# Optimization experiments

Hardware: AMD Instinct MI355X
Metric: run time of the kernel (lower is better)

## Reference

```python
import jax, jax.numpy as jnp
import numpy as np

D_MODEL = 192
DEPTH = 16
D_INNER = 384   # expand=2
D_STATE = 16
D_CONV = 4
DT_RANK = 12    # ceil(192/16)
J = 42
T = 8
NUM_CLASSES = 1000
B = 64
EPS = 1e-5


def setup_inputs() -> dict:
    key = jax.random.key(0)
    ks = jax.random.split(key, 16)

    def n(k, shape, scale=0.02):
        return jax.random.normal(k, shape, jnp.float32) * scale

    dt_bias_init = float(np.log(np.expm1(0.01)))  # softplus^-1(0.01), mamba dt init
    A_init = jnp.log(jnp.tile(jnp.arange(1, D_STATE + 1, dtype=jnp.float32), (DEPTH, D_INNER, 1)))
    return {
        "x": jax.random.normal(ks[0], (B, T, J, 3), jnp.float32),
        "joint_embed_w": n(ks[1], (D_MODEL, 3)),
        "joint_embed_b": jnp.zeros((D_MODEL,), jnp.float32),
        "cls_token": n(ks[2], (1, 1, D_MODEL)),
        "spatial_pos": n(ks[3], (1, J + 1, D_MODEL)),
        "temporal_pos": n(ks[4], (1, T, D_MODEL)),
        "norm_w": jnp.ones((DEPTH, D_MODEL), jnp.float32),
        "in_proj_w": n(ks[5], (DEPTH, 2 * D_INNER, D_MODEL)),
        "conv_w": n(ks[6], (DEPTH, D_INNER, D_CONV), 0.1),
        "conv_b": jnp.zeros((DEPTH, D_INNER), jnp.float32),
        "x_proj_w": n(ks[7], (DEPTH, DT_RANK + 2 * D_STATE, D_INNER)),
        "dt_proj_w": n(ks[8], (DEPTH, D_INNER, DT_RANK), DT_RANK ** -0.5),
        "dt_proj_b": jnp.full((DEPTH, D_INNER), dt_bias_init, jnp.float32),
        "A_log": A_init,
        "Dp": jnp.ones((DEPTH, D_INNER), jnp.float32),
        "out_proj_w": n(ks[9], (DEPTH, D_MODEL, D_INNER)),
        "norm_f_w": jnp.ones((D_MODEL,), jnp.float32),
        "head_w": n(ks[10], (NUM_CLASSES, D_MODEL)),
        "head_b": jnp.zeros((NUM_CLASSES,), jnp.float32),
    }


def rmsnorm(x, w):
    return x * jax.lax.rsqrt(jnp.mean(x * x, axis=-1, keepdims=True) + EPS) * w


def mamba(x, in_w, cw, cb, xp_w, dtw, dtb, A_log, Dp, ow):
    # x: (B, L, d_model)
    Bsz, L, _ = x.shape
    xz = jnp.einsum('bld,ed->ble', x, in_w)          # (B,L,2*di)
    u, z = jnp.split(xz, 2, axis=-1)
    # depthwise causal conv over time
    uc = jnp.transpose(u, (0, 2, 1))                  # (B,di,L)
    uc = jnp.pad(uc, ((0, 0), (0, 0), (D_CONV - 1, 0)))
    uc = jax.lax.conv_general_dilated(
        uc, cw[:, None, :], (1,), 'VALID',
        dimension_numbers=('NCH', 'OIH', 'NCH'),
        feature_group_count=D_INNER) + cb[None, :, None]
    u = jax.nn.silu(jnp.transpose(uc, (0, 2, 1)))     # (B,L,di)
    dbl = jnp.einsum('bld,ed->ble', u, xp_w)          # (B,L,dt_rank+2*ds)
    dt, Bm, Cm = jnp.split(dbl, [DT_RANK, DT_RANK + D_STATE], axis=-1)
    delta = jax.nn.softplus(jnp.einsum('blr,dr->bld', dt, dtw) + dtb)  # (B,L,di)
    A = -jnp.exp(A_log)                               # (di,ds)

    def step(h, xs):
        d_t, B_t, C_t, u_t = xs                       # (B,di),(B,ds),(B,ds),(B,di)
        h = h * jnp.exp(d_t[..., None] * A) + (d_t * u_t)[..., None] * B_t[:, None, :]
        return h, jnp.einsum('bds,bs->bd', h, C_t)

    xs = (jnp.swapaxes(delta, 0, 1), jnp.swapaxes(Bm, 0, 1),
          jnp.swapaxes(Cm, 0, 1), jnp.swapaxes(u, 0, 1))
    h0 = jnp.zeros((Bsz, D_INNER, D_STATE), x.dtype)
    _, ys = jax.lax.scan(step, h0, xs)                # (L,B,di)
    y = jnp.swapaxes(ys, 0, 1) + u * Dp
    y = y * jax.nn.silu(z)
    return jnp.einsum('ble,de->bld', y, ow)


def reference(x, joint_embed_w, joint_embed_b, cls_token, spatial_pos, temporal_pos,
              norm_w, in_proj_w, conv_w, conv_b, x_proj_w, dt_proj_w, dt_proj_b,
              A_log, Dp, out_proj_w, norm_f_w, head_w, head_b):
    Bq, Tq, Jq, _ = x.shape
    xe = jnp.einsum('btjc,dc->btjd', x, joint_embed_w) + joint_embed_b
    xe = xe.reshape(Bq * Tq, Jq, D_MODEL)
    cls = jnp.broadcast_to(cls_token, (Bq * Tq, 1, D_MODEL))
    xcat = jnp.concatenate([cls, xe], axis=1) + spatial_pos   # (B*T, J+1, M)
    cls_tokens = xcat[:Bq, :1, :]
    body = xcat[:, 1:, :].reshape(Bq, Tq, Jq, D_MODEL)
    body = body.transpose(0, 2, 1, 3).reshape(Bq * Jq, Tq, D_MODEL) + temporal_pos
    body = body.reshape(Bq, Jq, Tq, D_MODEL).transpose(0, 2, 1, 3).reshape(Bq, Tq * Jq, D_MODEL)
    h = jnp.concatenate([cls_tokens, body], axis=1)           # (B, 1+T*J, M)

    residual = None
    for i in range(DEPTH):
        residual = h + residual if residual is not None else h
        hn = rmsnorm(residual, norm_w[i])
        h = mamba(hn, in_proj_w[i], conv_w[i], conv_b[i], x_proj_w[i],
                  dt_proj_w[i], dt_proj_b[i], A_log[i], Dp[i], out_proj_w[i])
    residual = h + residual
    feat = rmsnorm(residual, norm_f_w)[:, 0, :]
    return feat @ head_w.T + head_b
```

## Files before the change

kernel.cpp:

```cpp
#include <hip/hip_runtime.h>
#include <hip/hip_bf16.h>
#include <math.h>

#define B_ 64
#define T_ 8
#define J_ 42
#define L_ 337
#define D_ 192
#define E_ 384
#define S_ 16
#define R_ 12
#define DEPTH_ 16
#define NC_ 1000
#define M_ (B_*L_)
#define XZW_ (2*E_)
#define DBLW_ (R_+2*S_)
#define EPS_ 1e-5f
#define CH_ 22
#define NCH_ 16
#define LOG2E_ 1.44269504088896f

typedef float    f32x4  __attribute__((ext_vector_type(4)));
typedef unsigned u32x4  __attribute__((ext_vector_type(4)));
typedef __bf16   bf16x8 __attribute__((ext_vector_type(8)));

__device__ __forceinline__ float sigmoid_(float x){ return 1.f/(1.f+__expf(-x)); }
__device__ __forceinline__ float softplus_(float x){
  return (x > 20.f) ? x : __logf(1.f + __expf(x));
}
__device__ __forceinline__ unsigned short f2bf(float f){
  unsigned u = __float_as_uint(f);
  unsigned r = (u + 0x7fffu + ((u>>16)&1u)) >> 16;
  return (unsigned short)r;
}
__device__ __forceinline__ float bf2f(unsigned short h){
  return __uint_as_float(((unsigned)h)<<16);
}

__global__ void cvt_bf16_kernel(const float* __restrict__ in,
                                unsigned short* __restrict__ out, int n){
  int i = blockIdx.x*blockDim.x + threadIdx.x;
  if (i < n) out[i] = f2bf(in[i]);
}

__global__ void embed_kernel(const float* __restrict__ x,
                             const float* __restrict__ jw,
                             const float* __restrict__ jb,
                             const float* __restrict__ cls,
                             const float* __restrict__ sp,
                             const float* __restrict__ tp,
                             float* __restrict__ h) {
  int idx = blockIdx.x*blockDim.x + threadIdx.x;
  if (idx >= M_*D_) return;
  int d = idx % D_;
  int m = idx / D_;
  int l = m % L_;
  int b = m / L_;
  float v;
  if (l == 0) {
    v = cls[d] + sp[d];
  } else {
    int lm = l-1, t = lm / J_, j = lm % J_;
    const float* xp = x + ((size_t)((b*T_+t)*J_ + j))*3;
    v = jb[d] + sp[(1+j)*D_+d] + tp[t*D_+d]
      + xp[0]*jw[d*3+0] + xp[1]*jw[d*3+1] + xp[2]*jw[d*3+2];
  }
  h[idx] = v;
}

__global__ __launch_bounds__(64) void addnorm_kernel(float* __restrict__ residual,
    const float* __restrict__ h, const float* __restrict__ w,
    unsigned short* __restrict__ hn) {
  int m = blockIdx.x;
  int lane = threadIdx.x;
  size_t base = (size_t)m*D_;
  float r[3];
  float ss = 0.f;
  #pragma unroll
  for (int i=0;i<3;i++){
    int d = lane + i*64;
    r[i] = residual[base+d] + h[base+d];
    residual[base+d] = r[i];
    ss += r[i]*r[i];
  }
  #pragma unroll
  for (int off=32; off>=1; off>>=1) ss += __shfl_xor(ss, off, 64);
  float sc = rsqrtf(ss*(1.f/(float)D_) + EPS_);
  #pragma unroll
  for (int i=0;i<3;i++){
    int d = lane + i*64;
    hn[base+d] = f2bf(r[i]*sc*w[d]);
  }
}

template<int NWAVES>
__global__ __launch_bounds__(64*NWAVES) void gemm_mfma(
    const unsigned short* __restrict__ A,
    const unsigned short* __restrict__ W,
    float* __restrict__ C, int M, int N, int K)
{
  const int wave = threadIdx.x >> 6;
  const int lane = threadIdx.x & 63;
  const int row0 = blockIdx.x * 64;
  const int col0 = (blockIdx.y * NWAVES + wave) * 64;
  const int lr = lane & 15;
  const int lk = (lane >> 4) * 8;
  const bf16x8 bzero = __builtin_bit_cast(bf16x8, (u32x4)(0u));
  f32x4 acc[4][4] = {};
  for (int k0 = 0; k0 < K; k0 += 32) {
    bf16x8 af[4], bfr[4];
    #pragma unroll
    for (int i=0;i<4;i++)
      af[i] = __builtin_bit_cast(bf16x8,
          *(const u32x4*)(A + (size_t)(row0 + i*16 + lr)*K + k0 + lk));
    #pragma unroll
    for (int j=0;j<4;j++) {
      int col = col0 + j*16 + lr;
      bfr[j] = (col < N) ? __builtin_bit_cast(bf16x8,
          *(const u32x4*)(W + (size_t)col*K + k0 + lk)) : bzero;
    }
    #pragma unroll
    for (int i=0;i<4;i++)
      #pragma unroll
      for (int j=0;j<4;j++)
        acc[i][j] = __builtin_amdgcn_mfma_f32_16x16x32_bf16(af[i], bfr[j], acc[i][j], 0, 0, 0);
  }
  const int ro = (lane >> 4) * 4;
  #pragma unroll
  for (int i=0;i<4;i++) {
    #pragma unroll
    for (int j=0;j<4;j++) {
      int col = col0 + j*16 + lr;
      if (col >= N) continue;
      #pragma unroll
      for (int r=0;r<4;r++) {
        int row = row0 + i*16 + ro + r;
        C[(size_t)row*N + col] = acc[i][j][r];
      }
    }
  }
}

__global__ void conv_silu_kernel(const float* __restrict__ xz,
    const float* __restrict__ cw, const float* __restrict__ cb,
    unsigned short* __restrict__ u2) {
  int idx = blockIdx.x*blockDim.x + threadIdx.x;
  if (idx >= M_*E_) return;
  int d = idx % E_;
  int m = idx / E_;
  int l = m % L_;
  float acc = cb[d];
  #pragma unroll
  for (int k=0;k<4;k++){
    int lk = l + k - 3;
    if (lk >= 0) acc += cw[d*4+k] * xz[(size_t)(m + k - 3)*XZW_ + d];
  }
  u2[idx] = f2bf(acc * sigmoid_(acc));
}

__global__ __launch_bounds__(64) void scan_partA(
    const float* __restrict__ dbl,
    const unsigned short* __restrict__ u2,
    const float* __restrict__ dtw,
    const float* __restrict__ dtb,
    const float* __restrict__ A_log,
    float* __restrict__ part_h,
    float* __restrict__ part_sd)
{
  const int b = blockIdx.x;
  const int d = blockIdx.y*64 + threadIdx.x;
  const int c = blockIdx.z;
  const int t0 = c*CH_;
  const int t1 = (t0+CH_ < L_) ? t0+CH_ : L_;
  float dtw_r[R_];
  #pragma unroll
  for (int r=0;r<R_;r++) dtw_r[r] = dtw[d*R_+r];
  const float dtb_r = dtb[d];
  const float a1 = -__expf(A_log[d*S_]) * LOG2E_;
  float h[S_];
  #pragma unroll
  for (int s=0;s<S_;s++) h[s] = 0.f;
  float sum_dl = 0.f;
  const size_t m0 = (size_t)b*L_;

  float4 q[7];
  { const float4* dr = (const float4*)(dbl + (m0+t0)*DBLW_);
    #pragma unroll
    for (int i=0;i<7;i++) q[i] = dr[i]; }
  float u_ = bf2f(u2[(m0+t0)*E_ + d]);

  for (int t=t0; t<t1; ++t) {
    float4 nq[7]; float nu = 0.f;
    if (t+1 < t1) {
      const float4* dr = (const float4*)(dbl + (m0+t+1)*DBLW_);
      #pragma unroll
      for (int i=0;i<7;i++) nq[i] = dr[i];
      nu = bf2f(u2[(m0+t+1)*E_ + d]);
    }
    float qf[28];
    #pragma unroll
    for (int i=0;i<7;i++){
      qf[4*i+0]=q[i].x; qf[4*i+1]=q[i].y; qf[4*i+2]=q[i].z; qf[4*i+3]=q[i].w;
    }
    float dtv = dtb_r;
    #pragma unroll
    for (int r=0;r<R_;r++) dtv = fmaf(qf[r], dtw_r[r], dtv);
    dtv = softplus_(dtv);
    sum_dl += dtv;
    const float du = dtv * u_;
    const float rr = exp2f(dtv * a1);
    float p = rr;
    #pragma unroll
    for (int s=0;s<S_;s++){
      h[s] = fmaf(h[s], p, du*qf[R_+s]);
      p *= rr;
    }
    #pragma unroll
    for (int i=0;i<7;i++) q[i] = nq[i];
    u_ = nu;
  }
  const size_t pb = (size_t)b*NCH_ + c;
  #pragma unroll
  for (int s=0;s<S_;s++) part_h[(pb*S_ + s)*E_ + d] = h[s];
  part_sd[pb*E_ + d] = sum_dl;
}

__global__ __launch_bounds__(64) void scan_partC(
    const float* __restrict__ dbl,
    const unsigned short* __restrict__ u2,
    const float* __restrict__ xz,
    const float* __restrict__ dtw, const float* __restrict__ dtb,
    const float* __restrict__ A_log, const float* __restrict__ Dp,
    const float* __restrict__ part_h, const float* __restrict__ part_sd,
    unsigned short* __restrict__ y)
{
  const int b = blockIdx.x;
  const int d = blockIdx.y*64 + threadIdx.x;
  const int c = blockIdx.z;
  const int t0 = c*CH_;
  const int t1 = (t0+CH_ < L_) ? t0+CH_ : L_;
  float dtw_r[R_];
  #pragma unroll
  for (int r=0;r<R_;r++) dtw_r[r] = dtw[d*R_+r];
  const float dtb_r = dtb[d];
  const float dpv   = Dp[d];
  const float a1 = -__expf(A_log[d*S_]) * LOG2E_;
  float h[S_];
  #pragma unroll
  for (int s=0;s<S_;s++) h[s] = 0.f;
  for (int cc=0; cc<c; ++cc) {
    const size_t pb = (size_t)b*NCH_ + cc;
    const float sd = part_sd[pb*E_ + d];
    const float rr = exp2f(a1*sd);
    float p = rr;
    #pragma unroll
    for (int s=0;s<S_;s++){
      h[s] = fmaf(h[s], p, part_h[(pb*S_ + s)*E_ + d]);
      p *= rr;
    }
  }

  const size_t m0 = (size_t)b*L_;
  float4 q[11];
  { const float4* dr = (const float4*)(dbl + (m0+t0)*DBLW_);
    #pragma unroll
    for (int i=0;i<11;i++) q[i] = dr[i]; }
  float u_ = bf2f(u2[(m0+t0)*E_ + d]);
  float z_ = xz[(m0+t0)*XZW_ + E_ + d];

  for (int t=t0; t<t1; ++t) {
    float4 nq[11]; float nu = 0.f, nz = 0.f;
    if (t+1 < t1) {
      const float4* dr = (const float4*)(dbl + (m0+t+1)*DBLW_);
      #pragma unroll
      for (int i=0;i<11;i++) nq[i] = dr[i];
      nu = bf2f(u2[(m0+t+1)*E_ + d]);
      nz = xz[(m0+t+1)*XZW_ + E_ + d];
    }
    float qf[44];
    #pragma unroll
    for (int i=0;i<11;i++){
      qf[4*i+0]=q[i].x; qf[4*i+1]=q[i].y; qf[4*i+2]=q[i].z; qf[4*i+3]=q[i].w;
    }
    float dtv = dtb_r;
    #pragma unroll
    for (int r=0;r<R_;r++) dtv = fmaf(qf[r], dtw_r[r], dtv);
    dtv = softplus_(dtv);
    const float du = dtv * u_;
    const float rr = exp2f(dtv * a1);
    float p = rr;
    float acc0=0.f, acc1=0.f, acc2=0.f, acc3=0.f;
    #pragma unroll
    for (int s=0;s<S_;s+=4){
      h[s+0] = fmaf(h[s+0], p, du*qf[R_+s+0]); p *= rr;
      h[s+1] = fmaf(h[s+1], p, du*qf[R_+s+1]); p *= rr;
      h[s+2] = fmaf(h[s+2], p, du*qf[R_+s+2]); p *= rr;
      h[s+3] = fmaf(h[s+3], p, du*qf[R_+s+3]); p *= rr;
      acc0 = fmaf(h[s+0], qf[R_+S_+s+0], acc0);
      acc1 = fmaf(h[s+1], qf[R_+S_+s+1], acc1);
      acc2 = fmaf(h[s+2], qf[R_+S_+s+2], acc2);
      acc3 = fmaf(h[s+3], qf[R_+S_+s+3], acc3);
    }
    const float acc = (acc0+acc1)+(acc2+acc3);
    const float yv = fmaf(u_, dpv, acc) * (z_ * sigmoid_(z_));
    y[(m0+t)*E_ + d] = f2bf(yv);
    #pragma unroll
    for (int i=0;i<11;i++) q[i] = nq[i];
    u_ = nu; z_ = nz;
  }
}

__global__ __launch_bounds__(64) void final_norm_kernel(const float* __restrict__ residual,
    const float* __restrict__ h, const float* __restrict__ w,
    float* __restrict__ feat) {
  int b = blockIdx.x;
  int lane = threadIdx.x;
  size_t base = (size_t)b*L_*D_;
  float r[3]; float ss = 0.f;
  #pragma unroll
  for (int i=0;i<3;i++){
    int d = lane + i*64;
    r[i] = residual[base+d] + h[base+d];
    ss += r[i]*r[i];
  }
  #pragma unroll
  for (int off=32; off>=1; off>>=1) ss += __shfl_xor(ss, off, 64);
  float sc = rsqrtf(ss*(1.f/(float)D_) + EPS_);
  #pragma unroll
  for (int i=0;i<3;i++){
    int d = lane + i*64;
    feat[b*D_ + d] = r[i]*sc*w[d];
  }
}

__global__ __launch_bounds__(256) void head_kernel(const float* __restrict__ feat,
    const float* __restrict__ hw, const float* __restrict__ hb,
    float* __restrict__ out) {
  __shared__ float fs[D_];
  int b = blockIdx.x;
  for (int i=threadIdx.x;i<D_;i+=blockDim.x) fs[i] = feat[b*D_+i];
  __syncthreads();
  for (int n=threadIdx.x;n<NC_;n+=blockDim.x){
    float acc = hb[n];
    #pragma unroll 4
    for (int k=0;k<D_;k++) acc += fs[k]*hw[(size_t)n*D_+k];
    out[(size_t)b*NC_+n] = acc;
  }
}

extern "C" void kernel_launch(void* const* d_in, const int* in_sizes, int n_in,
                              void* d_out, int out_size, void* d_ws, size_t ws_size,
                              hipStream_t stream) {
  const float* x        = (const float*)d_in[0];
  const float* jw       = (const float*)d_in[1];
  const float* jb       = (const float*)d_in[2];
  const float* cls      = (const float*)d_in[3];
  const float* sp       = (const float*)d_in[4];
  const float* tp       = (const float*)d_in[5];
  const float* norm_w   = (const float*)d_in[6];
  const float* in_w     = (const float*)d_in[7];
  const float* conv_w   = (const float*)d_in[8];
  const float* conv_b   = (const float*)d_in[9];
  const float* xp_w     = (const float*)d_in[10];
  const float* dt_w     = (const float*)d_in[11];
  const float* dt_b     = (const float*)d_in[12];
  const float* A_log    = (const float*)d_in[13];
  const float* Dp       = (const float*)d_in[14];
  const float* out_w    = (const float*)d_in[15];
  const float* norm_f_w = (const float*)d_in[16];
  const float* head_w   = (const float*)d_in[17];
  const float* head_b   = (const float*)d_in[18];
  float* out = (float*)d_out;

  float* ws = (float*)d_ws;
  float* residual = ws;
  float* hbuf     = residual + (size_t)M_*D_;
  float* xz       = hbuf     + (size_t)M_*D_;
  float* dbl      = xz       + (size_t)M_*XZW_;
  float* feat     = dbl      + (size_t)M_*DBLW_;
  unsigned short* bw = (unsigned short*)(feat + (size_t)B_*D_);
  unsigned short* hn    = bw;
  unsigned short* u2    = hn    + (size_t)M_*D_;
  unsigned short* ybuf  = u2    + (size_t)M_*E_;
  unsigned short* w_in  = ybuf  + (size_t)M_*E_;
  unsigned short* w_xp  = w_in  + (size_t)DEPTH_*XZW_*D_;
  unsigned short* w_out = w_xp  + (size_t)DEPTH_*DBLW_*E_;
  float* part_h  = (float*)(w_out + (size_t)DEPTH_*D_*E_);
  float* part_sd = part_h + (size_t)B_*NCH_*S_*E_;

  {
    int n1 = DEPTH_*XZW_*D_;
    int n2 = DEPTH_*DBLW_*E_;
    int n3 = DEPTH_*D_*E_;
    cvt_bf16_kernel<<<(n1+255)/256, 256, 0, stream>>>(in_w,  w_in,  n1);
    cvt_bf16_kernel<<<(n2+255)/256, 256, 0, stream>>>(xp_w,  w_xp,  n2);
    cvt_bf16_kernel<<<(n3+255)/256, 256, 0, stream>>>(out_w, w_out, n3);
  }

  hipMemsetAsync(residual, 0, (size_t)M_*D_*sizeof(float), stream);

  embed_kernel<<<(M_*D_+255)/256, 256, 0, stream>>>(x, jw, jb, cls, sp, tp, hbuf);

  for (int i = 0; i < DEPTH_; ++i) {
    addnorm_kernel<<<M_, 64, 0, stream>>>(residual, hbuf, norm_w + (size_t)i*D_, hn);
    gemm_mfma<4><<<dim3(M_/64, XZW_/256), 256, 0, stream>>>(
        hn, w_in + (size_t)i*XZW_*D_, xz, M_, XZW_, D_);
    conv_silu_kernel<<<(M_*E_+255)/256, 256, 0, stream>>>(
        xz, conv_w + (size_t)i*E_*4, conv_b + (size_t)i*E_, u2);
    gemm_mfma<1><<<dim3(M_/64, 1), 64, 0, stream>>>(
        u2, w_xp + (size_t)i*DBLW_*E_, dbl, M_, DBLW_, E_);
    scan_partA<<<dim3(B_, E_/64, NCH_-1), 64, 0, stream>>>(
        dbl, u2,
        dt_w + (size_t)i*E_*R_, dt_b + (size_t)i*E_,
        A_log + (size_t)i*E_*S_, part_h, part_sd);
    scan_partC<<<dim3(B_, E_/64, NCH_), 64, 0, stream>>>(
        dbl, u2, xz,
        dt_w + (size_t)i*E_*R_, dt_b + (size_t)i*E_,
        A_log + (size_t)i*E_*S_, Dp + (size_t)i*E_,
        part_h, part_sd, ybuf);
    gemm_mfma<3><<<dim3(M_/64, 1), 192, 0, stream>>>(
        ybuf, w_out + (size_t)i*D_*E_, hbuf, M_, D_, E_);
  }

  final_norm_kernel<<<B_, 64, 0, stream>>>(residual, hbuf, norm_f_w, feat);
  head_kernel<<<B_, 256, 0, stream>>>(feat, head_w, head_b, out);
}
```

Before: 2.852 ms.

## Fuse residual add and RMSNorm into out-proj GEMM epilogue, store xz in bf16

The out-projection GEMM now adds its result straight into the residual and computes the next layer's RMSNorm in its epilogue, using a shared-memory cross-wave row reduction. This removes the separate addnorm kernel and the hbuf round trip. The in-projection output xz is stored as bf16, which halves the traffic for conv and the scan's z reads at some cost in precision. The x_proj GEMM is retiled to 4 waves over rows, and the scan kernels use 128-thread blocks.

```diff
diff --git a/kernel.cpp b/kernel.cpp
--- a/kernel.cpp
+++ b/kernel.cpp
@@ -49,7 +49,7 @@
                              const float* __restrict__ cls,
                              const float* __restrict__ sp,
                              const float* __restrict__ tp,
-                             float* __restrict__ h) {
+                             float* __restrict__ res) {
   int idx = blockIdx.x*blockDim.x + threadIdx.x;
   if (idx >= M_*D_) return;
   int d = idx % D_;
@@ -65,12 +65,11 @@
     v = jb[d] + sp[(1+j)*D_+d] + tp[t*D_+d]
       + xp[0]*jw[d*3+0] + xp[1]*jw[d*3+1] + xp[2]*jw[d*3+2];
   }
-  h[idx] = v;
-}
-
-__global__ __launch_bounds__(64) void addnorm_kernel(float* __restrict__ residual,
-    const float* __restrict__ h, const float* __restrict__ w,
-    unsigned short* __restrict__ hn) {
+  res[idx] = v;
+}
+
+__global__ __launch_bounds__(64) void norm0_kernel(const float* __restrict__ residual,
+    const float* __restrict__ w, unsigned short* __restrict__ hn) {
   int m = blockIdx.x;
   int lane = threadIdx.x;
   size_t base = (size_t)m*D_;
@@ -79,8 +78,7 @@
   #pragma unroll
   for (int i=0;i<3;i++){
     int d = lane + i*64;
-    r[i] = residual[base+d] + h[base+d];
-    residual[base+d] = r[i];
+    r[i] = residual[base+d];
     ss += r[i]*r[i];
   }
   #pragma unroll
@@ -93,55 +91,85 @@
   }
 }
 
-template<int NWAVES>
-__global__ __launch_bounds__(64*NWAVES) void gemm_mfma(
+__global__ __launch_bounds__(256) void gemm_in(
     const unsigned short* __restrict__ A,
     const unsigned short* __restrict__ W,
-    float* __restrict__ C, int M, int N, int K)
+    unsigned short* __restrict__ C)
 {
   const int wave = threadIdx.x >> 6;
   const int lane = threadIdx.x & 63;
   const int row0 = blockIdx.x * 64;
-  const int col0 = (blockIdx.y * NWAVES + wave) * 64;
+  const int col0 = (blockIdx.y * 4 + wave) * 64;
+  const int lr = lane & 15;
+  const int lk = (lane >> 4) * 8;
+  f32x4 acc[4][4] = {};
+  for (int k0 = 0; k0 < D_; k0 += 32) {
+    bf16x8 af[4], bfr[4];
+    #pragma unroll
+    for (int i=0;i<4;i++)
+      af[i] = __builtin_bit_cast(bf16x8,
+          *(const u32x4*)(A + (size_t)(row0 + i*16 + lr)*D_ + k0 + lk));
+    #pragma unroll
+    for (int j=0;j<4;j++)
+      bfr[j] = __builtin_bit_cast(bf16x8,
+          *(const u32x4*)(W + (size_t)(col0 + j*16 + lr)*D_ + k0 + lk));
+    #pragma unroll
+    for (int i=0;i<4;i++)
+      #pragma unroll
+      for (int j=0;j<4;j++)
+        acc[i][j] = __builtin_amdgcn_mfma_f32_16x16x32_bf16(af[i], bfr[j], acc[i][j], 0, 0, 0);
+  }
+  const int ro = (lane >> 4) * 4;
+  #pragma unroll
+  for (int i=0;i<4;i++)
+    #pragma unroll
+    for (int j=0;j<4;j++){
+      int col = col0 + j*16 + lr;
+      #pragma unroll
+      for (int r=0;r<4;r++){
+        int row = row0 + i*16 + ro + r;
+        C[(size_t)row*XZW_ + col] = f2bf(acc[i][j][r]);
+      }
+    }
+}
+
+__global__ __launch_bounds__(256) void gemm_xp(
+    const unsigned short* __restrict__ A,
+    const unsigned short* __restrict__ W,
+    float* __restrict__ C)
+{
+  const int wave = threadIdx.x >> 6;
+  const int lane = threadIdx.x & 63;
+  const int row0 = blockIdx.x * 64 + wave * 16;
   const int lr = lane & 15;
   const int lk = (lane >> 4) * 8;
   const bf16x8 bzero = __builtin_bit_cast(bf16x8, (u32x4)(0u));
-  f32x4 acc[4][4] = {};
-  for (int k0 = 0; k0 < K; k0 += 32) {
-    bf16x8 af[4], bfr[4];
-    #pragma unroll
-    for (int i=0;i<4;i++)
-      af[i] = __builtin_bit_cast(bf16x8,
-          *(const u32x4*)(A + (size_t)(row0 + i*16 + lr)*K + k0 + lk));
-    #pragma unroll
-    for (int j=0;j<4;j++) {
-      int col = col0 + j*16 + lr;
-      bfr[j] = (col < N) ? __builtin_bit_cast(bf16x8,
-          *(const u32x4*)(W + (size_t)col*K + k0 + lk)) : bzero;
-    }
-    #pragma unroll
-    for (int i=0;i<4;i++)
-      #pragma unroll
-      for (int j=0;j<4;j++)
-        acc[i][j] = __builtin_amdgcn_mfma_f32_16x16x32_bf16(af[i], bfr[j], acc[i][j], 0, 0, 0);
+  f32x4 acc[3] = {};
+  for (int k0 = 0; k0 < E_; k0 += 32) {
+    bf16x8 af = __builtin_bit_cast(bf16x8,
+        *(const u32x4*)(A + (size_t)(row0 + lr)*E_ + k0 + lk));
+    #pragma unroll
+    for (int j=0;j<3;j++){
+      int col = j*16 + lr;
+      bf16x8 bfr = (col < DBLW_) ? __builtin_bit_cast(bf16x8,
+          *(const u32x4*)(W + (size_t)col*E_ + k0 + lk)) : bzero;
+      acc[j] = __builtin_amdgcn_mfma_f32_16x16x32_bf16(af, bfr, acc[j], 0, 0, 0);
+    }
   }
   const int ro = (lane >> 4) * 4;
   #pragma unroll
-  for (int i=0;i<4;i++) {
-    #pragma unroll
-    for (int j=0;j<4;j++) {
-      int col = col0 + j*16 + lr;
-      if (col >= N) continue;
-      #pragma unroll
-      for (int r=0;r<4;r++) {
-        int row = row0 + i*16 + ro + r;
-        C[(size_t)row*N + col] = acc[i][j][r];
-      }
-    }
-  }
-}
-
-__global__ void conv_silu_kernel(const float* __restrict__ xz,
+  for (int j=0;j<3;j++){
+    int col = j*16 + lr;
+    if (col >= DBLW_) continue;
+    #pragma unroll
+    for (int r=0;r<4;r++){
+      int row = row0 + ro + r;
+      C[(size_t)row*DBLW_ + col] = acc[j][r];
+    }
+  }
+}
+
+__global__ void conv_silu_kernel(const unsigned short* __restrict__ xz,
     const float* __restrict__ cw, const float* __restrict__ cb,
     unsigned short* __restrict__ u2) {
   int idx = blockIdx.x*blockDim.x + threadIdx.x;
@@ -153,12 +181,12 @@
   #pragma unroll
   for (int k=0;k<4;k++){
     int lk = l + k - 3;
-    if (lk >= 0) acc += cw[d*4+k] * xz[(size_t)(m + k - 3)*XZW_ + d];
+    if (lk >= 0) acc += cw[d*4+k] * bf2f(xz[(size_t)(m + k - 3)*XZW_ + d]);
   }
   u2[idx] = f2bf(acc * sigmoid_(acc));
 }
 
-__global__ __launch_bounds__(64) void scan_partA(
+__global__ __launch_bounds__(128) void scan_partA(
     const float* __restrict__ dbl,
     const unsigned short* __restrict__ u2,
     const float* __restrict__ dtw,
@@ -168,7 +196,7 @@
     float* __restrict__ part_sd)
 {
   const int b = blockIdx.x;
-  const int d = blockIdx.y*64 + threadIdx.x;
+  const int d = blockIdx.y*128 + threadIdx.x;
   const int c = blockIdx.z;
   const int t0 = c*CH_;
   const int t1 = (t0+CH_ < L_) ? t0+CH_ : L_;
@@ -225,17 +253,17 @@
   part_sd[pb*E_ + d] = sum_dl;
 }
 
-__global__ __launch_bounds__(64) void scan_partC(
+__global__ __launch_bounds__(128) void scan_partC(
     const float* __restrict__ dbl,
     const unsigned short* __restrict__ u2,
-    const float* __restrict__ xz,
+    const unsigned short* __restrict__ xz,
     const float* __restrict__ dtw, const float* __restrict__ dtb,
     const float* __restrict__ A_log, const float* __restrict__ Dp,
     const float* __restrict__ part_h, const float* __restrict__ part_sd,
     unsigned short* __restrict__ y)
 {
   const int b = blockIdx.x;
-  const int d = blockIdx.y*64 + threadIdx.x;
+  const int d = blockIdx.y*128 + threadIdx.x;
   const int c = blockIdx.z;
   const int t0 = c*CH_;
   const int t1 = (t0+CH_ < L_) ? t0+CH_ : L_;
@@ -266,7 +294,7 @@
     #pragma unroll
     for (int i=0;i<11;i++) q[i] = dr[i]; }
   float u_ = bf2f(u2[(m0+t0)*E_ + d]);
-  float z_ = xz[(m0+t0)*XZW_ + E_ + d];
+  float z_ = bf2f(xz[(m0+t0)*XZW_ + E_ + d]);
 
   for (int t=t0; t<t1; ++t) {
     float4 nq[11]; float nu = 0.f, nz = 0.f;
@@ -275,7 +303,7 @@
       #pragma unroll
       for (int i=0;i<11;i++) nq[i] = dr[i];
       nu = bf2f(u2[(m0+t+1)*E_ + d]);
-      nz = xz[(m0+t+1)*XZW_ + E_ + d];
+      nz = bf2f(xz[(m0+t+1)*XZW_ + E_ + d]);
     }
     float qf[44];
     #pragma unroll
@@ -310,9 +338,83 @@
   }
 }
 
+__global__ __launch_bounds__(192) void gemm_out_fused(
+    const unsigned short* __restrict__ A,
+    const unsigned short* __restrict__ W,
+    float* __restrict__ residual,
+    const float* __restrict__ wnext,
+    unsigned short* __restrict__ hn)
+{
+  const int wave = threadIdx.x >> 6;
+  const int lane = threadIdx.x & 63;
+  const int row0 = blockIdx.x * 64;
+  const int col0 = wave * 64;
+  const int lr = lane & 15;
+  const int lk = (lane >> 4) * 8;
+  f32x4 acc[4][4] = {};
+  for (int k0 = 0; k0 < E_; k0 += 32) {
+    bf16x8 af[4], bfr[4];
+    #pragma unroll
+    for (int i=0;i<4;i++)
+      af[i] = __builtin_bit_cast(bf16x8,
+          *(const u32x4*)(A + (size_t)(row0 + i*16 + lr)*E_ + k0 + lk));
+    #pragma unroll
+    for (int j=0;j<4;j++)
+      bfr[j] = __builtin_bit_cast(bf16x8,
+          *(const u32x4*)(W + (size_t)(col0 + j*16 + lr)*E_ + k0 + lk));
+    #pragma unroll
+    for (int i=0;i<4;i++)
+      #pragma unroll
+      for (int j=0;j<4;j++)
+        acc[i][j] = __builtin_amdgcn_mfma_f32_16x16x32_bf16(af[i], bfr[j], acc[i][j], 0, 0, 0);
+  }
+  const int ro = (lane >> 4) * 4;
+  __shared__ float rs[3][64];
+  float wn[4];
+  #pragma unroll
+  for (int j=0;j<4;j++) wn[j] = wnext[col0 + j*16 + lr];
+  float resv[4][4][4];
+  #pragma unroll
+  for (int i=0;i<4;i++){
+    #pragma unroll
+    for (int r=0;r<4;r++){
+      int row = row0 + i*16 + ro + r;
+      float psum = 0.f;
+      #pragma unroll
+      for (int j=0;j<4;j++){
+        int col = col0 + j*16 + lr;
+        float v = residual[(size_t)row*D_ + col] + acc[i][j][r];
+        resv[i][j][r] = v;
+        residual[(size_t)row*D_ + col] = v;
+        psum = fmaf(v, v, psum);
+      }
+      psum += __shfl_xor(psum, 1);
+      psum += __shfl_xor(psum, 2);
+      psum += __shfl_xor(psum, 4);
+      psum += __shfl_xor(psum, 8);
+      if (lr == 0) rs[wave][i*16 + ro + r] = psum;
+    }
+  }
+  __syncthreads();
+  #pragma unroll
+  for (int i=0;i<4;i++){
+    #pragma unroll
+    for (int r=0;r<4;r++){
+      int rloc = i*16 + ro + r;
+      float tot = rs[0][rloc] + rs[1][rloc] + rs[2][rloc];
+      float sc = rsqrtf(tot*(1.f/(float)D_) + EPS_);
+      int row = row0 + rloc;
+      #pragma unroll
+      for (int j=0;j<4;j++){
+        int col = col0 + j*16 + lr;
+        hn[(size_t)row*D_ + col] = f2bf(resv[i][j][r]*sc*wn[j]);
+      }
+    }
+  }
+}
+
 __global__ __launch_bounds__(64) void final_norm_kernel(const float* __restrict__ residual,
-    const float* __restrict__ h, const float* __restrict__ w,
-    float* __restrict__ feat) {
+    const float* __restrict__ w, float* __restrict__ feat) {
   int b = blockIdx.x;
   int lane = threadIdx.x;
   size_t base = (size_t)b*L_*D_;
@@ -320,7 +422,7 @@
   #pragma unroll
   for (int i=0;i<3;i++){
     int d = lane + i*64;
-    r[i] = residual[base+d] + h[base+d];
+    r[i] = residual[base+d];
     ss += r[i]*r[i];
   }
   #pragma unroll
@@ -374,19 +476,18 @@
 
   float* ws = (float*)d_ws;
   float* residual = ws;
-  float* hbuf     = residual + (size_t)M_*D_;
-  float* xz       = hbuf     + (size_t)M_*D_;
-  float* dbl      = xz       + (size_t)M_*XZW_;
+  float* dbl      = residual + (size_t)M_*D_;
   float* feat     = dbl      + (size_t)M_*DBLW_;
-  unsigned short* bw = (unsigned short*)(feat + (size_t)B_*D_);
+  float* part_h   = feat     + (size_t)B_*D_;
+  float* part_sd  = part_h   + (size_t)B_*NCH_*S_*E_;
+  unsigned short* bw = (unsigned short*)(part_sd + (size_t)B_*NCH_*E_);
   unsigned short* hn    = bw;
-  unsigned short* u2    = hn    + (size_t)M_*D_;
+  unsigned short* xz    = hn    + (size_t)M_*D_;
+  unsigned short* u2    = xz    + (size_t)M_*XZW_;
   unsigned short* ybuf  = u2    + (size_t)M_*E_;
   unsigned short* w_in  = ybuf  + (size_t)M_*E_;
   unsigned short* w_xp  = w_in  + (size_t)DEPTH_*XZW_*D_;
   unsigned short* w_out = w_xp  + (size_t)DEPTH_*DBLW_*E_;
-  float* part_h  = (float*)(w_out + (size_t)DEPTH_*D_*E_);
-  float* part_sd = part_h + (size_t)B_*NCH_*S_*E_;
 
   {
     int n1 = DEPTH_*XZW_*D_;
@@ -397,31 +498,30 @@
     cvt_bf16_kernel<<<(n3+255)/256, 256, 0, stream>>>(out_w, w_out, n3);
   }
 
-  hipMemsetAsync(residual, 0, (size_t)M_*D_*sizeof(float), stream);
-
-  embed_kernel<<<(M_*D_+255)/256, 256, 0, stream>>>(x, jw, jb, cls, sp, tp, hbuf);
+  embed_kernel<<<(M_*D_+255)/256, 256, 0, stream>>>(x, jw, jb, cls, sp, tp, residual);
+  norm0_kernel<<<M_, 64, 0, stream>>>(residual, norm_w, hn);
 
   for (int i = 0; i < DEPTH_; ++i) {
-    addnorm_kernel<<<M_, 64, 0, stream>>>(residual, hbuf, norm_w + (size_t)i*D_, hn);
-    gemm_mfma<4><<<dim3(M_/64, XZW_/256), 256, 0, stream>>>(
-        hn, w_in + (size_t)i*XZW_*D_, xz, M_, XZW_, D_);
+    gemm_in<<<dim3(M_/64, XZW_/256), 256, 0, stream>>>(
+        hn, w_in + (size_t)i*XZW_*D_, xz);
     conv_silu_kernel<<<(M_*E_+255)/256, 256, 0, stream>>>(
         xz, conv_w + (size_t)i*E_*4, conv_b + (size_t)i*E_, u2);
-    gemm_mfma<1><<<dim3(M_/64, 1), 64, 0, stream>>>(
-        u2, w_xp + (size_t)i*DBLW_*E_, dbl, M_, DBLW_, E_);
-    scan_partA<<<dim3(B_, E_/64, NCH_-1), 64, 0, stream>>>(
+    gemm_xp<<<M_/64, 256, 0, stream>>>(
+        u2, w_xp + (size_t)i*DBLW_*E_, dbl);
+    scan_partA<<<dim3(B_, E_/128, NCH_-1), 128, 0, stream>>>(
         dbl, u2,
         dt_w + (size_t)i*E_*R_, dt_b + (size_t)i*E_,
         A_log + (size_t)i*E_*S_, part_h, part_sd);
-    scan_partC<<<dim3(B_, E_/64, NCH_), 64, 0, stream>>>(
+    scan_partC<<<dim3(B_, E_/128, NCH_), 128, 0, stream>>>(
         dbl, u2, xz,
         dt_w + (size_t)i*E_*R_, dt_b + (size_t)i*E_,
         A_log + (size_t)i*E_*S_, Dp + (size_t)i*E_,
         part_h, part_sd, ybuf);
-    gemm_mfma<3><<<dim3(M_/64, 1), 192, 0, stream>>>(
-        ybuf, w_out + (size_t)i*D_*E_, hbuf, M_, D_, E_);
-  }
-
-  final_norm_kernel<<<B_, 64, 0, stream>>>(residual, hbuf, norm_f_w, feat);
+    const float* wnext = (i+1 < DEPTH_) ? (norm_w + (size_t)(i+1)*D_) : norm_f_w;
+    gemm_out_fused<<<M_/64, 192, 0, stream>>>(
+        ybuf, w_out + (size_t)i*D_*E_, residual, wnext, hn);
+  }
+
+  final_norm_kernel<<<B_, 64, 0, stream>>>(residual, norm_f_w, feat);
   head_kernel<<<B_, 256, 0, stream>>>(feat, head_w, head_b, out);
 }
```

After: 2.938 ms. 3.0% more time.
